# Performance work log

Hardware: AMD Instinct MI355X
Metric: run time of the kernel (lower is better)

## Reference

```python
import jax, jax.numpy as jnp
import numpy as np

# ---- static sizes ----
B, N, F_IN = 256, 512, 128          # graphs, nodes-per-graph, node feature dim
LATENT = [128, 128, 128, 128]        # per-layer GNN widths (conv_params)
D = sum(LATENT)                      # dense_dim = 512
OUT = 128                            # output_dim
DEG = 16                             # avg degree -> edges per node
TN = B * N                           # 131072 total nodes
E = TN * DEG                         # 2097152 directed edges


def setup_inputs() -> dict:
    key = jax.random.key(0)
    ks = jax.random.split(key, 10)
    node_feat = jax.random.normal(ks[0], (TN, F_IN), dtype=jnp.float32)
    # edges are intra-graph: global node id = graph_base + local id in [0, N)
    base = jnp.repeat(jnp.arange(B, dtype=jnp.int32) * N, N * DEG)  # [E]
    edge_src = base + jax.random.randint(ks[1], (E,), 0, N, dtype=jnp.int32)
    edge_dst = base + jax.random.randint(ks[2], (E,), 0, N, dtype=jnp.int32)
    conv_W = jax.random.normal(ks[3], (len(LATENT), 128, 128), dtype=jnp.float32) * 0.08
    conv_b = jnp.zeros((len(LATENT), 128), dtype=jnp.float32)
    att_W = jax.random.normal(ks[4], (D, D), dtype=jnp.float32) * 0.04
    att_b = jnp.zeros((D,), dtype=jnp.float32)
    att_v = jax.random.normal(ks[5], (D,), dtype=jnp.float32) * 0.06
    out_W = jax.random.normal(ks[6], (D, OUT), dtype=jnp.float32) * 0.06
    out_b = jnp.zeros((OUT,), dtype=jnp.float32)
    return {"node_feat": node_feat, "edge_src": edge_src, "edge_dst": edge_dst,
            "conv_W": conv_W, "conv_b": conv_b, "att_W": att_W, "att_b": att_b,
            "att_v": att_v, "out_W": out_W, "out_b": out_b}


def reference(node_feat, edge_src, edge_dst, conv_W, conv_b, att_W, att_b, att_v, out_W, out_b):
    # node_degs = degree + 1 (n2n row sums + 1), matching graph.degs + 1
    ones = jnp.ones((E,), dtype=node_feat.dtype)
    degs = jax.ops.segment_sum(ones, edge_dst, num_segments=TN) + 1.0   # [TN]
    degs = degs[:, None]

    # graph convolution layers: spmm(A, h) + h -> Linear -> /deg -> tanh
    h = node_feat
    layers = []
    for l in range(len(LATENT)):
        agg = jax.ops.segment_sum(h[edge_src], edge_dst, num_segments=TN) + h  # [TN, d]
        lin = agg @ conv_W[l] + conv_b[l]
        h = jnp.tanh(lin / degs)
        layers.append(h)
    cat = jnp.concatenate(layers, axis=1)        # [TN, D]

    # per-graph additive attention pooling (FlexAddAttention aggregation)
    x = cat.reshape(B, N, D)                     # uniform graph sizes
    scores = jnp.einsum('bnd,d->bn', jnp.tanh(x @ att_W + att_b), att_v)  # [B, N]
    attn = jax.nn.softmax(scores, axis=1)
    pooled = jnp.einsum('bn,bnd->bd', attn, x)   # [B, D]

    # out_params + relu (second relu in original is idempotent)
    return jax.nn.relu(pooled @ out_W + out_b)   # [B, OUT]
```

## Files before the change

kernel.cpp:

```cpp
#include <hip/hip_runtime.h>
#include <hip/hip_bf16.h>

#define TN 131072
#define NB 256
#define NN 512
#define FD 128
#define DD 512
#define NE 2097152
#define NEB 8192
#define NL 4
#define PITCH 136
#define CHK 32
#define NCH 16
#define CICAP 576

typedef __attribute__((ext_vector_type(8))) short bf16x8;
typedef __attribute__((ext_vector_type(4))) float f32x4;

__device__ __forceinline__ float b2f(unsigned int u) {
    union { unsigned int i; float f; } c; c.i = u << 16; return c.f;
}
__device__ __forceinline__ unsigned short f2b(float f) {
    union { float f; unsigned int i; } c; c.f = f;
    unsigned int x = c.i;
    return (unsigned short)((x + 0x7fffu + ((x >> 16) & 1u)) >> 16);
}
__device__ __forceinline__ void add2(float& a0, float& a1, unsigned int v) {
    union { unsigned int u; float f; } lo, hi;
    lo.u = v << 16; hi.u = v & 0xffff0000u;
    a0 += lo.f; a1 += hi.f;
}
__device__ __forceinline__ void set2(float& a0, float& a1, unsigned int v) {
    union { unsigned int u; float f; } lo, hi;
    lo.u = v << 16; hi.u = v & 0xffff0000u;
    a0 = lo.f; a1 = hi.f;
}
__device__ __forceinline__ uint4 packv8(const float* a) {
    uint4 p;
    p.x = (unsigned int)f2b(a[0]) | ((unsigned int)f2b(a[1]) << 16);
    p.y = (unsigned int)f2b(a[2]) | ((unsigned int)f2b(a[3]) << 16);
    p.z = (unsigned int)f2b(a[4]) | ((unsigned int)f2b(a[5]) << 16);
    p.w = (unsigned int)f2b(a[6]) | ((unsigned int)f2b(a[7]) << 16);
    return p;
}
__device__ __forceinline__ float ftanh(float x) {
    float xc = fminf(fmaxf(x, -9.0f), 9.0f);
    float e = __expf(2.0f * xc);
    return (e - 1.0f) * __builtin_amdgcn_rcpf(e + 1.0f);
}
__device__ __forceinline__ void gl_lds16(const unsigned short* g, unsigned short* l) {
    __builtin_amdgcn_global_load_lds(
        (const __attribute__((address_space(1))) unsigned int*)g,
        (__attribute__((address_space(3))) unsigned int*)l,
        16, 0, 0);
}
__device__ __forceinline__ void dot2acc(float& acc, unsigned int p, unsigned int ones) {
    asm("v_dot2_f32_bf16 %0, %1, %2, %0" : "+v"(acc) : "v"(p), "v"(ones));
}

__global__ __launch_bounds__(1024) void csr_b_k(
    const int* __restrict__ src, const int* __restrict__ dst,
    int* __restrict__ row_ptr, int* __restrict__ col_off,
    float* __restrict__ degs)
{
    __shared__ int cnt[NN];
    __shared__ int ss[NN];
    int b = blockIdx.x, t = threadIdx.x;
    int e0 = b * NEB;
    if (t < NN) cnt[t] = 0;
    __syncthreads();
    #pragma unroll
    for (int i = 0; i < NEB / 1024; i++) {
        int d = dst[e0 + t + i * 1024] & (NN - 1);
        atomicAdd(&cnt[d], 1);
    }
    __syncthreads();
    int c = 0;
    if (t < NN) { c = cnt[t]; ss[t] = c; }
    __syncthreads();
    for (int off = 1; off < NN; off <<= 1) {
        int v = (t < NN && t >= off) ? ss[t - off] : 0;
        __syncthreads();
        if (t < NN) ss[t] += v;
        __syncthreads();
    }
    if (t < NN) {
        int excl = ss[t] - c;
        int gid = b * NN + t;
        row_ptr[gid] = e0 + excl;
        degs[gid] = (float)(c + 1);
        cnt[t] = excl;
        if (b == NB - 1 && t == NN - 1) row_ptr[TN] = NE;
    }
    __syncthreads();
    #pragma unroll
    for (int i = 0; i < NEB / 1024; i++) {
        int e = e0 + t + i * 1024;
        int d = dst[e] & (NN - 1);
        int p = atomicAdd(&cnt[d], 1);
        col_off[e0 + p] = (src[e] & (NN - 1)) * (PITCH * 2);
    }
}

__global__ __launch_bounds__(256) void prep_k(const float* __restrict__ attW,
                                              const float* __restrict__ convW,
                                              unsigned short* __restrict__ attWt,
                                              unsigned short* __restrict__ convWt) {
    __shared__ float tile[32][33];
    int z = blockIdx.z;
    int tx = threadIdx.x & 31, ty = threadIdx.x >> 5;
    if (z == 0) {
        int k0 = blockIdx.x * 32, n0 = blockIdx.y * 32;
        #pragma unroll
        for (int i = 0; i < 32; i += 8)
            tile[ty + i][tx] = attW[(size_t)(k0 + ty + i) * DD + n0 + tx];
        __syncthreads();
        #pragma unroll
        for (int i = 0; i < 32; i += 8)
            attWt[(size_t)(n0 + ty + i) * DD + k0 + tx] = f2b(tile[tx][ty + i]);
    } else {
        if (blockIdx.x >= FD / 32 || blockIdx.y >= FD / 32) return;
        const float* Wl = convW + (size_t)(z - 1) * FD * FD;
        unsigned short* Wtl = convWt + (size_t)(z - 1) * FD * FD;
        int f0 = blockIdx.x * 32, o0 = blockIdx.y * 32;
        #pragma unroll
        for (int i = 0; i < 32; i += 8)
            tile[ty + i][tx] = Wl[(size_t)(f0 + ty + i) * FD + o0 + tx];
        __syncthreads();
        #pragma unroll
        for (int i = 0; i < 32; i += 8)
            Wtl[(size_t)(o0 + ty + i) * FD + f0 + tx] = f2b(tile[tx][ty + i]);
    }
}

__global__ __launch_bounds__(1024) void conv_all_k(
    const float* __restrict__ node_feat,
    const unsigned short* __restrict__ Wt,
    const float* __restrict__ bias,
    const int* __restrict__ rp, const int* __restrict__ coff,
    const float* __restrict__ degs,
    unsigned short* __restrict__ cat)
{
    __shared__ unsigned short hW[NN * PITCH];
    __shared__ unsigned short agg[2][CHK * PITCH];
    __shared__ int ciL[2][CICAP];
    __shared__ int rpL[NN + 1];
    const int tid = threadIdx.x;
    const int g0 = blockIdx.x * NN;
    const int lane = tid & 63, w = tid >> 6;
    const int lr = lane & 15, lh = lane >> 4;
    const int mo = w >> 1, nd = w & 1;
    const int gn = tid >> 5;
    const int gs = tid & 31;
    const char* hWb = (const char*)hW;
    const unsigned int SEL0 = 0x01000504u;
    const unsigned int SEL1 = 0x03020706u;
    const unsigned int ONES = 0x3F803F80u;

    if (tid <= NN) rpL[tid] = rp[g0 + tid];

    #pragma unroll
    for (int i = 0; i < 8; i++) {
        int u = tid + i * 1024;
        int row = u >> 4, cu = u & 15;
        const float4* s4 = (const float4*)(node_feat + (size_t)(g0 + row) * FD + cu * 8);
        float4 x = s4[0], y = s4[1];
        float tmp[8] = {x.x, x.y, x.z, x.w, y.x, y.y, y.z, y.w};
        *(uint4*)&hW[row * PITCH + cu * 8] = packv8(tmp);
    }
    __syncthreads();

    auto do_gather = [&](int nl, int rs, int re, int eb, const int* cib,
                         unsigned short* buf) {
        const char* rowb = hWb + nl * (PITCH * 2);
        uint2 v = *(const uint2*)(rowb + gs * 8);
        float a0, a1, a2, a3;
        set2(a0, a1, v.x); set2(a2, a3, v.y);
        int r1 = re;
        int rlim = eb + CICAP; if (r1 > rlim) r1 = rlim;
        int j = rs;
        for (; j + 8 <= r1; j += 8) {
            int off[8];
            #pragma unroll
            for (int i = 0; i < 8; i++) off[i] = cib[j - eb + i];
            uint2 u[8];
            #pragma unroll
            for (int i = 0; i < 8; i++) u[i] = *(const uint2*)(hWb + off[i] + gs * 8);
            #pragma unroll
            for (int i = 0; i < 4; i++) {
                unsigned int x1 = u[2 * i].x, x2 = u[2 * i + 1].x;
                unsigned int y1 = u[2 * i].y, y2 = u[2 * i + 1].y;
                dot2acc(a0, __builtin_amdgcn_perm(x1, x2, SEL0), ONES);
                dot2acc(a1, __builtin_amdgcn_perm(x1, x2, SEL1), ONES);
                dot2acc(a2, __builtin_amdgcn_perm(y1, y2, SEL0), ONES);
                dot2acc(a3, __builtin_amdgcn_perm(y1, y2, SEL1), ONES);
            }
        }
        for (; j + 2 <= r1; j += 2) {
            int o0 = cib[j - eb], o1 = cib[j - eb + 1];
            uint2 u0 = *(const uint2*)(hWb + o0 + gs * 8);
            uint2 u1 = *(const uint2*)(hWb + o1 + gs * 8);
            dot2acc(a0, __builtin_amdgcn_perm(u0.x, u1.x, SEL0), ONES);
            dot2acc(a1, __builtin_amdgcn_perm(u0.x, u1.x, SEL1), ONES);
            dot2acc(a2, __builtin_amdgcn_perm(u0.y, u1.y, SEL0), ONES);
            dot2acc(a3, __builtin_amdgcn_perm(u0.y, u1.y, SEL1), ONES);
        }
        if (j < r1) {
            int off = cib[j - eb];
            uint2 u = *(const uint2*)(hWb + off + gs * 8);
            add2(a0, a1, u.x); add2(a2, a3, u.y);
            j = r1;
        }
        for (; j < re; j++) {
            int off = coff[j];
            uint2 u = *(const uint2*)(hWb + off + gs * 8);
            add2(a0, a1, u.x); add2(a2, a3, u.y);
        }
        uint2 pk;
        pk.x = (unsigned int)f2b(a0) | ((unsigned int)f2b(a1) << 16);
        pk.y = (unsigned int)f2b(a2) | ((unsigned int)f2b(a3) << 16);
        *(uint2*)&buf[gn * PITCH + gs * 4] = pk;
    };

    for (int l = 0; l < NL; l++) {
        bf16x8 af[4];
        #pragma unroll
        for (int ks = 0; ks < 4; ks++)
            af[ks] = *(const bf16x8*)&Wt[((size_t)l * FD + mo * 16 + lr) * FD + ks * 32 + lh * 8];
        float4 bs = *(const float4*)&bias[l * FD + mo * 16 + lh * 4];

        {
            int eb0 = rpL[0];
            int cnt0 = rpL[CHK] - eb0;          if (cnt0 > CICAP) cnt0 = CICAP;
            int eb1 = rpL[CHK];
            int cnt1 = rpL[2 * CHK] - eb1;      if (cnt1 > CICAP) cnt1 = CICAP;
            int rs0 = rpL[gn], re0 = rpL[gn + 1];
            if (tid < cnt0) ciL[0][tid] = coff[eb0 + tid];
            if (tid < cnt1) ciL[1][tid] = coff[eb1 + tid];
            __syncthreads();
            do_gather(gn, rs0, re0, eb0, ciL[0], agg[0]);
        }
        __syncthreads();

        for (int c = 0; c < NCH; c++) {
            int cur = c & 1;
            int rs_n = 0, re_n = 0, eb_n = 0;
            if (c < NCH - 1) {
                eb_n = rpL[(c + 1) * CHK];
                rs_n = rpL[(c + 1) * CHK + gn];
                re_n = rpL[(c + 1) * CHK + gn + 1];
            }
            int scnt = 0, sval = 0;
            if (c <= NCH - 3) {
                int eb2 = rpL[(c + 2) * CHK];
                scnt = rpL[(c + 3) * CHK] - eb2; if (scnt > CICAP) scnt = CICAP;
                if (tid < scnt) sval = coff[eb2 + tid];
            }
            f32x4 cc = (f32x4){0.f, 0.f, 0.f, 0.f};
            {
                const unsigned short* ab = &agg[cur][(nd * 16 + lr) * PITCH + lh * 8];
                #pragma unroll
                for (int ks = 0; ks < 4; ks++) {
                    bf16x8 bfv = *(const bf16x8*)&ab[ks * 32];
                    cc = __builtin_amdgcn_mfma_f32_16x16x32_bf16(af[ks], bfv, cc, 0, 0, 0);
                }
            }
            {
                int dstl = c * CHK + nd * 16 + lr;
                float rd = __builtin_amdgcn_rcpf(degs[g0 + dstl]);
                float t0 = ftanh((cc[0] + bs.x) * rd);
                float t1 = ftanh((cc[1] + bs.y) * rd);
                float t2 = ftanh((cc[2] + bs.z) * rd);
                float t3 = ftanh((cc[3] + bs.w) * rd);
                uint2 pk;
                pk.x = (unsigned int)f2b(t0) | ((unsigned int)f2b(t1) << 16);
                pk.y = (unsigned int)f2b(t2) | ((unsigned int)f2b(t3) << 16);
                *(uint2*)&cat[(size_t)(g0 + dstl) * DD + l * FD + mo * 16 + lh * 4] = pk;
            }
            if (tid < scnt) ciL[cur][tid] = sval;
            if (c < NCH - 1)
                do_gather((c + 1) * CHK + gn, rs_n, re_n, eb_n, ciL[(c + 1) & 1], agg[cur ^ 1]);
            __syncthreads();
        }

        if (l < NL - 1) {
            #pragma unroll
            for (int i = 0; i < 8; i++) {
                int u = tid + i * 1024;
                int row = u >> 4, cu = u & 15;
                uint4 v = *(const uint4*)&cat[(size_t)(g0 + row) * DD + l * FD + cu * 8];
                *(uint4*)&hW[row * PITCH + cu * 8] = v;
            }
            __syncthreads();
        }
    }
}

__global__ __launch_bounds__(256) void scores_k(
    const unsigned short* __restrict__ X,
    const unsigned short* __restrict__ Wt,
    const float* __restrict__ bv, const float* __restrict__ vv,
    float* __restrict__ sp)
{
    __shared__ unsigned short sXl[128 * 64];
    __shared__ unsigned short sWl[128 * 64];
    int bid = blockIdx.x;
    int swz = (bid & 7) * 512 + (bid >> 3);
    int bx = swz >> 2, by = swz & 3;
    int tid = threadIdx.x;
    int lane = tid & 63, wid = tid >> 6;
    int wm = wid >> 1, wn = wid & 1;
    int m0 = bx * 128;
    int n0 = by * 128;
    int lr = lane & 15, lh = lane >> 4;

    f32x4 acc[4][4];
    #pragma unroll
    for (int mi = 0; mi < 4; mi++)
        #pragma unroll
        for (int ni = 0; ni < 4; ni++)
            acc[mi][ni] = (f32x4){0.f, 0.f, 0.f, 0.f};

    for (int k0 = 0; k0 < DD; k0 += 64) {
        __syncthreads();
        #pragma unroll
        for (int i = 0; i < 4; i++) {
            int u = (i << 8) + tid;
            int row = u >> 3, cu = u & 7;
            int su = cu ^ (row & 7);
            gl_lds16(&X[(size_t)(m0 + row) * DD + k0 + su * 8], &sXl[u * 8]);
            gl_lds16(&Wt[(size_t)(n0 + row) * DD + k0 + su * 8], &sWl[u * 8]);
        }
        __syncthreads();
        #pragma unroll
        for (int kk = 0; kk < 64; kk += 32) {
            int cu0 = (kk >> 3) + lh;
            bf16x8 afv[4], bfv[4];
            #pragma unroll
            for (int mi = 0; mi < 4; mi++) {
                int rr = wm * 64 + mi * 16 + lr;
                afv[mi] = *(const bf16x8*)&sXl[rr * 64 + ((cu0 ^ (rr & 7)) << 3)];
            }
            #pragma unroll
            for (int ni = 0; ni < 4; ni++) {
                int rr = wn * 64 + ni * 16 + lr;
                bfv[ni] = *(const bf16x8*)&sWl[rr * 64 + ((cu0 ^ (rr & 7)) << 3)];
            }
            #pragma unroll
            for (int mi = 0; mi < 4; mi++)
                #pragma unroll
                for (int ni = 0; ni < 4; ni++)
                    acc[mi][ni] = __builtin_amdgcn_mfma_f32_16x16x32_bf16(
                        afv[mi], bfv[ni], acc[mi][ni], 0, 0, 0);
        }
    }

    float vcol[4], bcol[4];
    #pragma unroll
    for (int ni = 0; ni < 4; ni++) {
        int col = n0 + wn * 64 + ni * 16 + lr;
        vcol[ni] = vv[col];
        bcol[ni] = bv[col];
    }
    #pragma unroll
    for (int mi = 0; mi < 4; mi++) {
        #pragma unroll
        for (int r = 0; r < 4; r++) {
            float part = 0.f;
            #pragma unroll
            for (int ni = 0; ni < 4; ni++)
                part += ftanh(acc[mi][ni][r] + bcol[ni]) * vcol[ni];
            part += __shfl_xor(part, 1);
            part += __shfl_xor(part, 2);
            part += __shfl_xor(part, 4);
            part += __shfl_xor(part, 8);
            if (lr == 0) {
                int row = m0 + wm * 64 + mi * 16 + lh * 4 + r;
                sp[(size_t)row * 8 + by * 2 + wn] = part;
            }
        }
    }
}

__global__ __launch_bounds__(512) void poolout_k(
    const float* __restrict__ sp, const unsigned short* __restrict__ X,
    const float* __restrict__ Wo, const float* __restrict__ bo,
    float* __restrict__ out)
{
    __shared__ float sattn[512];
    __shared__ float wmax[8];
    __shared__ float wsum[8];
    __shared__ float pred[3][512];
    __shared__ float pl[512];
    int b = blockIdx.x, t = threadIdx.x;
    int lane = t & 63, wid = t >> 6;

    float s;
    {
        const float4* p = (const float4*)&sp[((size_t)b * NN + t) * 8];
        float4 x = p[0], y = p[1];
        s = x.x + x.y + x.z + x.w + y.x + y.y + y.z + y.w;
    }
    float m = s;
    #pragma unroll
    for (int off = 1; off < 64; off <<= 1) m = fmaxf(m, __shfl_xor(m, off));
    if (lane == 0) wmax[wid] = m;
    __syncthreads();
    m = wmax[0];
    #pragma unroll
    for (int i = 1; i < 8; i++) m = fmaxf(m, wmax[i]);
    float e = expf(s - m);
    float ssum = e;
    #pragma unroll
    for (int off = 1; off < 64; off <<= 1) ssum += __shfl_xor(ssum, off);
    if (lane == 0) wsum[wid] = ssum;
    __syncthreads();
    float tot = wsum[0];
    #pragma unroll
    for (int i = 1; i < 8; i++) tot += wsum[i];
    sattn[t] = e * (1.0f / tot);
    __syncthreads();

    int rg = t >> 7, tc = t & 127;
    float4 acc = {0.f, 0.f, 0.f, 0.f};
    const unsigned short* Xb = X + (size_t)b * NN * DD;
    int n0 = rg * 128;
    #pragma unroll 4
    for (int n = n0; n < n0 + 128; n++) {
        float a = sattn[n];
        uint2 px = *(const uint2*)&Xb[(size_t)n * DD + tc * 4];
        acc.x += a * b2f(px.x & 0xffff);
        acc.y += a * b2f(px.x >> 16);
        acc.z += a * b2f(px.y & 0xffff);
        acc.w += a * b2f(px.y >> 16);
    }
    if (rg > 0) *(float4*)&pred[rg - 1][tc * 4] = acc;
    __syncthreads();
    if (rg == 0) {
        #pragma unroll
        for (int g = 0; g < 3; g++) {
            float4 q = *(const float4*)&pred[g][tc * 4];
            acc.x += q.x; acc.y += q.y; acc.z += q.z; acc.w += q.w;
        }
        *(float4*)&pl[tc * 4] = acc;
    }
    __syncthreads();

    if (t < 128) {
        float o = 0.f;
        #pragma unroll 8
        for (int k = 0; k < DD; k++) o += pl[k] * Wo[k * 128 + t];
        out[b * 128 + t] = fmaxf(o + bo[t], 0.f);
    }
}

extern "C" void kernel_launch(void* const* d_in, const int* in_sizes, int n_in,
                              void* d_out, int out_size, void* d_ws, size_t ws_size,
                              hipStream_t stream)
{
    const float* node_feat = (const float*)d_in[0];
    const int*   edge_src  = (const int*)d_in[1];
    const int*   edge_dst  = (const int*)d_in[2];
    const float* conv_W    = (const float*)d_in[3];
    const float* conv_b    = (const float*)d_in[4];
    const float* att_W     = (const float*)d_in[5];
    const float* att_b     = (const float*)d_in[6];
    const float* att_v     = (const float*)d_in[7];
    const float* out_W     = (const float*)d_in[8];
    const float* out_b     = (const float*)d_in[9];
    float* out = (float*)d_out;
    (void)in_sizes; (void)n_in; (void)out_size;

    char* ws = (char*)d_ws;
    size_t off = 0;
    auto alloc = [&](size_t bytes) {
        void* p = ws + off;
        off += (bytes + 255) & ~(size_t)255;
        return p;
    };
    unsigned short* cat   = (unsigned short*)alloc((size_t)TN * DD * 2);
    int*   row_ptr = (int*)alloc((size_t)(TN + 1) * 4);
    int*   col_off = (int*)alloc((size_t)NE * 4);
    float* degs    = (float*)alloc((size_t)TN * 4);
    float* sp      = (float*)alloc((size_t)TN * 8 * 4);
    unsigned short* attWt = (unsigned short*)alloc((size_t)DD * DD * 2);
    unsigned short* convWt = (unsigned short*)alloc((size_t)NL * FD * FD * 2);
    if (off > ws_size) return;

    csr_b_k<<<NB, 1024, 0, stream>>>(edge_src, edge_dst, row_ptr, col_off, degs);
    prep_k<<<dim3(DD / 32, DD / 32, 1 + NL), 256, 0, stream>>>(att_W, conv_W, attWt, convWt);

    conv_all_k<<<NB, 1024, 0, stream>>>(node_feat, convWt, conv_b,
                                        row_ptr, col_off, degs, cat);

    scores_k<<<4096, 256, 0, stream>>>(cat, attWt, att_b, att_v, sp);
    poolout_k<<<NB, 512, 0, stream>>>(sp, cat, out_W, out_b, out);
}
```

Before: 354.6 us.

## Fuse per-graph CSR build and conv weight conversion into conv kernel

Result: no change. 350.7 us (-1.1%).

```diff
diff --git a/kernel.cpp b/kernel.cpp
--- a/kernel.cpp
+++ b/kernel.cpp
@@ -58,87 +58,26 @@
     asm("v_dot2_f32_bf16 %0, %1, %2, %0" : "+v"(acc) : "v"(p), "v"(ones));
 }
 
-__global__ __launch_bounds__(1024) void csr_b_k(
-    const int* __restrict__ src, const int* __restrict__ dst,
-    int* __restrict__ row_ptr, int* __restrict__ col_off,
-    float* __restrict__ degs)
-{
-    __shared__ int cnt[NN];
-    __shared__ int ss[NN];
-    int b = blockIdx.x, t = threadIdx.x;
-    int e0 = b * NEB;
-    if (t < NN) cnt[t] = 0;
-    __syncthreads();
-    #pragma unroll
-    for (int i = 0; i < NEB / 1024; i++) {
-        int d = dst[e0 + t + i * 1024] & (NN - 1);
-        atomicAdd(&cnt[d], 1);
-    }
-    __syncthreads();
-    int c = 0;
-    if (t < NN) { c = cnt[t]; ss[t] = c; }
-    __syncthreads();
-    for (int off = 1; off < NN; off <<= 1) {
-        int v = (t < NN && t >= off) ? ss[t - off] : 0;
-        __syncthreads();
-        if (t < NN) ss[t] += v;
-        __syncthreads();
-    }
-    if (t < NN) {
-        int excl = ss[t] - c;
-        int gid = b * NN + t;
-        row_ptr[gid] = e0 + excl;
-        degs[gid] = (float)(c + 1);
-        cnt[t] = excl;
-        if (b == NB - 1 && t == NN - 1) row_ptr[TN] = NE;
-    }
-    __syncthreads();
-    #pragma unroll
-    for (int i = 0; i < NEB / 1024; i++) {
-        int e = e0 + t + i * 1024;
-        int d = dst[e] & (NN - 1);
-        int p = atomicAdd(&cnt[d], 1);
-        col_off[e0 + p] = (src[e] & (NN - 1)) * (PITCH * 2);
-    }
-}
-
-__global__ __launch_bounds__(256) void prep_k(const float* __restrict__ attW,
-                                              const float* __restrict__ convW,
-                                              unsigned short* __restrict__ attWt,
-                                              unsigned short* __restrict__ convWt) {
+__global__ __launch_bounds__(256) void prep_k(const float* __restrict__ W,
+                                              unsigned short* __restrict__ Wt) {
     __shared__ float tile[32][33];
-    int z = blockIdx.z;
+    int k0 = blockIdx.x * 32, n0 = blockIdx.y * 32;
     int tx = threadIdx.x & 31, ty = threadIdx.x >> 5;
-    if (z == 0) {
-        int k0 = blockIdx.x * 32, n0 = blockIdx.y * 32;
-        #pragma unroll
-        for (int i = 0; i < 32; i += 8)
-            tile[ty + i][tx] = attW[(size_t)(k0 + ty + i) * DD + n0 + tx];
-        __syncthreads();
-        #pragma unroll
-        for (int i = 0; i < 32; i += 8)
-            attWt[(size_t)(n0 + ty + i) * DD + k0 + tx] = f2b(tile[tx][ty + i]);
-    } else {
-        if (blockIdx.x >= FD / 32 || blockIdx.y >= FD / 32) return;
-        const float* Wl = convW + (size_t)(z - 1) * FD * FD;
-        unsigned short* Wtl = convWt + (size_t)(z - 1) * FD * FD;
-        int f0 = blockIdx.x * 32, o0 = blockIdx.y * 32;
-        #pragma unroll
-        for (int i = 0; i < 32; i += 8)
-            tile[ty + i][tx] = Wl[(size_t)(f0 + ty + i) * FD + o0 + tx];
-        __syncthreads();
-        #pragma unroll
-        for (int i = 0; i < 32; i += 8)
-            Wtl[(size_t)(o0 + ty + i) * FD + f0 + tx] = f2b(tile[tx][ty + i]);
-    }
+    #pragma unroll
+    for (int i = 0; i < 32; i += 8)
+        tile[ty + i][tx] = W[(size_t)(k0 + ty + i) * DD + n0 + tx];
+    __syncthreads();
+    #pragma unroll
+    for (int i = 0; i < 32; i += 8)
+        Wt[(size_t)(n0 + ty + i) * DD + k0 + tx] = f2b(tile[tx][ty + i]);
 }
 
 __global__ __launch_bounds__(1024) void conv_all_k(
     const float* __restrict__ node_feat,
-    const unsigned short* __restrict__ Wt,
+    const float* __restrict__ convW,
     const float* __restrict__ bias,
-    const int* __restrict__ rp, const int* __restrict__ coff,
-    const float* __restrict__ degs,
+    const int* __restrict__ src, const int* __restrict__ dst,
+    int* __restrict__ col_off,
     unsigned short* __restrict__ cat)
 {
     __shared__ unsigned short hW[NN * PITCH];
@@ -147,17 +86,53 @@
     __shared__ int rpL[NN + 1];
     const int tid = threadIdx.x;
     const int g0 = blockIdx.x * NN;
+    const int e0 = blockIdx.x * NEB;
     const int lane = tid & 63, w = tid >> 6;
     const int lr = lane & 15, lh = lane >> 4;
     const int mo = w >> 1, nd = w & 1;
     const int gn = tid >> 5;
     const int gs = tid & 31;
     const char* hWb = (const char*)hW;
+    const int* co = col_off + e0;
     const unsigned int SEL0 = 0x01000504u;
     const unsigned int SEL1 = 0x03020706u;
     const unsigned int ONES = 0x3F803F80u;
 
-    if (tid <= NN) rpL[tid] = rp[g0 + tid];
+    {
+        int* cnt = (int*)agg;
+        int* ss  = cnt + NN;
+        if (tid < NN) cnt[tid] = 0;
+        __syncthreads();
+        #pragma unroll
+        for (int i = 0; i < NEB / 1024; i++) {
+            int d = dst[e0 + tid + i * 1024] & (NN - 1);
+            atomicAdd(&cnt[d], 1);
+        }
+        __syncthreads();
+        int c = 0;
+        if (tid < NN) { c = cnt[tid]; ss[tid] = c; }
+        __syncthreads();
+        for (int off = 1; off < NN; off <<= 1) {
+            int v = (tid < NN && tid >= off) ? ss[tid - off] : 0;
+            __syncthreads();
+            if (tid < NN) ss[tid] += v;
+            __syncthreads();
+        }
+        if (tid < NN) {
+            int excl = ss[tid] - c;
+            rpL[tid] = excl;
+            cnt[tid] = excl;
+        }
+        if (tid == 0) rpL[NN] = NEB;
+        __syncthreads();
+        #pragma unroll
+        for (int i = 0; i < NEB / 1024; i++) {
+            int e = e0 + tid + i * 1024;
+            int d = dst[e] & (NN - 1);
+            int p = atomicAdd(&cnt[d], 1);
+            col_off[e0 + p] = (src[e] & (NN - 1)) * (PITCH * 2);
+        }
+    }
 
     #pragma unroll
     for (int i = 0; i < 8; i++) {
@@ -212,7 +187,7 @@
             j = r1;
         }
         for (; j < re; j++) {
-            int off = coff[j];
+            int off = co[j];
             uint2 u = *(const uint2*)(hWb + off + gs * 8);
             add2(a0, a1, u.x); add2(a2, a3, u.y);
         }
@@ -225,8 +200,12 @@
     for (int l = 0; l < NL; l++) {
         bf16x8 af[4];
         #pragma unroll
-        for (int ks = 0; ks < 4; ks++)
-            af[ks] = *(const bf16x8*)&Wt[((size_t)l * FD + mo * 16 + lr) * FD + ks * 32 + lh * 8];
+        for (int ks = 0; ks < 4; ks++) {
+            const float* Wl = convW + (size_t)l * FD * FD + (size_t)(ks * 32 + lh * 8) * FD + mo * 16 + lr;
+            #pragma unroll
+            for (int j = 0; j < 8; j++)
+                af[ks][j] = (short)f2b(Wl[(size_t)j * FD]);
+        }
         float4 bs = *(const float4*)&bias[l * FD + mo * 16 + lh * 4];
 
         {
@@ -235,8 +214,8 @@
             int eb1 = rpL[CHK];
             int cnt1 = rpL[2 * CHK] - eb1;      if (cnt1 > CICAP) cnt1 = CICAP;
             int rs0 = rpL[gn], re0 = rpL[gn + 1];
-            if (tid < cnt0) ciL[0][tid] = coff[eb0 + tid];
-            if (tid < cnt1) ciL[1][tid] = coff[eb1 + tid];
+            if (tid < cnt0) ciL[0][tid] = co[eb0 + tid];
+            if (tid < cnt1) ciL[1][tid] = co[eb1 + tid];
             __syncthreads();
             do_gather(gn, rs0, re0, eb0, ciL[0], agg[0]);
         }
@@ -254,7 +233,7 @@
             if (c <= NCH - 3) {
                 int eb2 = rpL[(c + 2) * CHK];
                 scnt = rpL[(c + 3) * CHK] - eb2; if (scnt > CICAP) scnt = CICAP;
-                if (tid < scnt) sval = coff[eb2 + tid];
+                if (tid < scnt) sval = co[eb2 + tid];
             }
             f32x4 cc = (f32x4){0.f, 0.f, 0.f, 0.f};
             {
@@ -267,7 +246,7 @@
             }
             {
                 int dstl = c * CHK + nd * 16 + lr;
-                float rd = __builtin_amdgcn_rcpf(degs[g0 + dstl]);
+                float rd = __builtin_amdgcn_rcpf((float)(rpL[dstl + 1] - rpL[dstl] + 1));
                 float t0 = ftanh((cc[0] + bs.x) * rd);
                 float t1 = ftanh((cc[1] + bs.y) * rd);
                 float t2 = ftanh((cc[2] + bs.z) * rd);
@@ -479,19 +458,15 @@
         return p;
     };
     unsigned short* cat   = (unsigned short*)alloc((size_t)TN * DD * 2);
-    int*   row_ptr = (int*)alloc((size_t)(TN + 1) * 4);
     int*   col_off = (int*)alloc((size_t)NE * 4);
-    float* degs    = (float*)alloc((size_t)TN * 4);
     float* sp      = (float*)alloc((size_t)TN * 8 * 4);
     unsigned short* attWt = (unsigned short*)alloc((size_t)DD * DD * 2);
-    unsigned short* convWt = (unsigned short*)alloc((size_t)NL * FD * FD * 2);
     if (off > ws_size) return;
 
-    csr_b_k<<<NB, 1024, 0, stream>>>(edge_src, edge_dst, row_ptr, col_off, degs);
-    prep_k<<<dim3(DD / 32, DD / 32, 1 + NL), 256, 0, stream>>>(att_W, conv_W, attWt, convWt);
-
-    conv_all_k<<<NB, 1024, 0, stream>>>(node_feat, convWt, conv_b,
-                                        row_ptr, col_off, degs, cat);
+    prep_k<<<dim3(DD / 32, DD / 32), 256, 0, stream>>>(att_W, attWt);
+
+    conv_all_k<<<NB, 1024, 0, stream>>>(node_feat, conv_W, conv_b,
+                                        edge_src, edge_dst, col_off, cat);
 
     scores_k<<<4096, 256, 0, stream>>>(cat, attWt, att_b, att_v, sp);
     poolout_k<<<NB, 512, 0, stream>>>(sp, cat, out_W, out_b, out);
```
